# Performance work log

Measured on AMD Instinct MI355X. Metric: run time of the kernel, lower is better.

Reference implementation:

```python
import jax, jax.numpy as jnp
import numpy as np

B, C, M, H, W = 4, 12, 2, 320, 320
TOL = 1e-6
MAX_ITER = 10


def to_c(t):
    # [..., 2] real -> complex
    return jax.lax.complex(t[..., 0], t[..., 1])


def to_r(t):
    return jnp.stack([jnp.real(t), jnp.imag(t)], axis=-1)


def fft2c(x):
    return jnp.fft.fft2(x, axes=(-2, -1), norm='ortho')


def ifft2c(x):
    return jnp.fft.ifft2(x, axes=(-2, -1), norm='ortho')


def A_op(x, sm, mk):
    # x: [B,M,H,W] complex, sm: [B,C,M,H,W] complex, mk: [B,C,H,W] real
    coil_imgs = jnp.sum(x[:, None] * sm, axis=2)  # [B,C,H,W]
    return fft2c(coil_imgs) * mk


def AT_op(y, sm, mk):
    img = ifft2c(y * mk)  # [B,C,H,W]
    return jnp.sum(jnp.conj(sm) * img[:, :, None], axis=1)  # [B,M,H,W]


def cg_solve(x0, Mop, tol=TOL, max_iter=MAX_ITER):
    b = x0.shape[0]
    x0x0 = jnp.sum(jnp.abs(x0.reshape(b, -1)) ** 2, axis=-1)  # [B] real

    def body(carry, _):
        x, r, p, rr = carry
        active = jnp.min(rr / x0x0) > tol  # tol check, gated like the while-loop
        q = Mop(p)
        pq = jnp.sum((p * jnp.conj(q)).reshape(b, -1), axis=-1)  # complexDot(p, q)
        alpha = rr.astype(x0.dtype) / pq  # complex_div(rr, <p,q>)
        a = alpha[:, None, None, None]
        x_new = x + a * p
        r_new = r - a * q
        rr_new = jnp.sum(jnp.abs(r_new.reshape(b, -1)) ** 2, axis=-1)
        beta = (rr_new / rr)[:, None, None, None].astype(x0.dtype)
        p_new = r_new + beta * p
        new = (x_new, r_new, p_new, rr_new)
        carry = jax.tree.map(lambda n, o: jnp.where(active, n, o), new, carry)
        return carry, None

    rr0 = jnp.sum(jnp.abs(x0.reshape(b, -1)) ** 2, axis=-1)
    init = (jnp.zeros_like(x0), x0, x0, rr0)
    (x, _, _, _), _ = jax.lax.scan(body, init, None, length=max_iter)
    return x


def setup_inputs() -> dict:
    key = jax.random.key(0)
    k1, k2, k3, k4 = jax.random.split(key, 4)
    x = jax.random.normal(k1, (B, M, H, W, 2), dtype=jnp.float32)
    y = jax.random.normal(k2, (B, C, H, W, 2), dtype=jnp.float32)
    smaps = jax.random.normal(k3, (B, C, M, H, W, 2), dtype=jnp.float32) * 0.2
    mask = jax.random.randint(k4, (B, C, H, W, 1), 0, 2).astype(jnp.float32)
    lambda_a = jnp.full((1,), 0.05, dtype=jnp.float32)
    return {"x": x, "y": y, "smaps": smaps, "mask": mask, "lambda_a": lambda_a}


def reference(x, y, smaps, mask, lambda_a):
    z = to_c(x)          # [B,M,H,W]
    yc = to_c(y)         # [B,C,H,W]
    sm = to_c(smaps)     # [B,C,M,H,W]
    mk = mask[..., 0]    # [B,C,H,W]
    lam = lambda_a[0]

    x0 = lam * AT_op(yc, sm, mk) + z

    def Mop(p):
        return lam * AT_op(A_op(p, sm, mk), sm, mk) + p

    return to_r(cg_solve(x0, Mop))
```

## Files before the change

### kernel.cpp

```cpp
#include <hip/hip_runtime.h>
#include <math.h>

#define NB 4
#define NC 12
#define NM 2
#define NN 320
#define NHW (NN*NN)
#define NBC (NB*NC)
#define CG_TOL 1e-6f
#define NITER 10
#define CBLK 400
#define QBLK 320
#define CPG 3
#define NG  4

#define TWO_PI_F 6.28318530717958647692f

typedef float2 c32;

__device__ __forceinline__ c32 cmul(c32 a, c32 b){ return make_float2(a.x*b.x - a.y*b.y, a.x*b.y + a.y*b.x); }
__device__ __forceinline__ c32 cmulj(c32 a, c32 b){ return make_float2(a.x*b.x + a.y*b.y, a.x*b.y - a.y*b.x); }
__device__ __forceinline__ c32 cadd(c32 a, c32 b){ return make_float2(a.x+b.x, a.y+b.y); }
__device__ __forceinline__ c32 csub(c32 a, c32 b){ return make_float2(a.x-b.x, a.y-b.y); }
__device__ __forceinline__ c32 cscale(c32 a, float s){ return make_float2(a.x*s, a.y*s); }

template<bool CONJ>
__device__ __forceinline__ c32 twmul(c32 a, c32 t){
  return CONJ ? make_float2(a.x*t.x + a.y*t.y, a.y*t.x - a.x*t.y)
              : make_float2(a.x*t.x - a.y*t.y, a.y*t.x + a.x*t.y);
}

__device__ __forceinline__ float wave_reduce_f(float v) {
  #pragma unroll
  for (int off = 32; off >= 1; off >>= 1) v += __shfl_xor(v, off, 64);
  return v;
}
__device__ __forceinline__ c32 wave_reduce_c(c32 v) {
  #pragma unroll
  for (int off = 32; off >= 1; off >>= 1) {
    v.x += __shfl_xor(v.x, off, 64);
    v.y += __shfl_xor(v.y, off, 64);
  }
  return v;
}

__global__ __launch_bounds__(256)
void twiddle_init(c32* __restrict__ T320, c32* __restrict__ T64)
{
  const int t = threadIdx.x;
  {
    float s, c; sincosf(TWO_PI_F * (float)t / 320.f, &s, &c);
    T320[t] = make_float2(c, s);
  }
  if (t < 32) {
    float s, c; sincosf(TWO_PI_F * (float)t / 64.f, &s, &c);
    T64[t] = make_float2(c, s);
  }
}

template<bool FWD>
__device__ __forceinline__ void radix5(c32 V[5]) {
  constexpr float C1 = 0.30901699437494745f;
  constexpr float S1 = 0.9510565162951535f;
  constexpr float C2 = -0.8090169943749475f;
  constexpr float S2 = 0.5877852522924731f;
  constexpr float sg = FWD ? -1.f : 1.f;
  const c32 w1 = make_float2(C1,  sg*S1);
  const c32 w2 = make_float2(C2,  sg*S2);
  const c32 w3 = make_float2(C2, -sg*S2);
  const c32 w4 = make_float2(C1, -sg*S1);
  c32 v0=V[0], v1=V[1], v2=V[2], v3=V[3], v4=V[4];
  V[0] = cadd(cadd(v0, v1), cadd(cadd(v2, v3), v4));
  V[1] = cadd(v0, cadd(cadd(cmul(v1,w1), cmul(v2,w2)), cadd(cmul(v3,w3), cmul(v4,w4))));
  V[2] = cadd(v0, cadd(cadd(cmul(v1,w2), cmul(v2,w4)), cadd(cmul(v3,w1), cmul(v4,w3))));
  V[3] = cadd(v0, cadd(cadd(cmul(v1,w3), cmul(v2,w1)), cadd(cmul(v3,w4), cmul(v4,w2))));
  V[4] = cadd(v0, cadd(cadd(cmul(v1,w4), cmul(v2,w3)), cadd(cmul(v3,w2), cmul(v4,w1))));
}

template<bool FWD>
__device__ __forceinline__ void fft320_one(c32 A[5], const c32 ct[4], const c32 tw[6], int lane)
{
  radix5<FWD>(A);
  #pragma unroll
  for (int k = 1; k < 5; ++k) A[k] = twmul<FWD>(A[k], ct[k-1]);
  #pragma unroll
  for (int s = 0; s < 6; ++s) {
    const int m = 32 >> s;
    const c32 w = tw[s];
    const bool up = (lane & m) != 0;
    c32 o[5];
    #pragma unroll
    for (int k = 0; k < 5; ++k) { o[k].x = __shfl_xor(A[k].x, m, 64); o[k].y = __shfl_xor(A[k].y, m, 64); }
    #pragma unroll
    for (int k = 0; k < 5; ++k) {
      c32 lo = cadd(A[k], o[k]);
      c32 hi = twmul<FWD>(csub(o[k], A[k]), w);
      A[k] = up ? hi : lo;
    }
  }
}

__device__ __forceinline__ void ifft320_dit(c32 A[5], const c32 ct[4], const c32 tw[6], int lane)
{
  #pragma unroll
  for (int s = 5; s >= 0; --s) {
    const int m = 32 >> s;
    const c32 w = tw[s];
    const bool up = (lane & m) != 0;
    #pragma unroll
    for (int k = 0; k < 5; ++k) {
      c32 t = up ? twmul<false>(A[k], w) : A[k];
      c32 o; o.x = __shfl_xor(t.x, m, 64); o.y = __shfl_xor(t.y, m, 64);
      A[k] = up ? csub(o, t) : cadd(t, o);
    }
  }
  #pragma unroll
  for (int k = 1; k < 5; ++k) A[k] = twmul<false>(A[k], ct[k-1]);
  radix5<false>(A);
}

#define LOAD_TWIDDLES \
  c32 ct[4], tw[6]; \
  _Pragma("unroll") for (int k_ = 0; k_ < 4; ++k_) ct[k_] = T320[(k_ + 1) * lane]; \
  _Pragma("unroll") for (int s_ = 0; s_ < 6; ++s_) tw[s_] = T64[(lane & ((32 >> s_) - 1)) << s_];

__global__ __launch_bounds__(512)
void setup_mask_ifft(const c32* __restrict__ in, c32* __restrict__ out,
                     const float* __restrict__ mask,
                     const c32* __restrict__ T320, const c32* __restrict__ T64)
{
  __shared__ c32 tile[8][NN + 2];
  const int tid = threadIdx.x, lane = tid & 63, wv = tid >> 6;
  const int bc = blockIdx.y, r0 = blockIdx.x * 8;
  LOAD_TWIDDLES
  const int rv6 = __brev((unsigned)lane) >> 26;
  const int row = r0 + wv;
  c32 A[5];
  #pragma unroll
  for (int j = 0; j < 5; ++j) {
    const size_t idx = ((size_t)bc * NN + row) * NN + lane + 64*j;
    A[j] = cscale(in[idx], mask[idx]);
  }
  fft320_one<false>(A, ct, tw, lane);
  #pragma unroll
  for (int k = 0; k < 5; ++k) tile[wv][k + 5*rv6] = A[k];
  __syncthreads();
  #pragma unroll
  for (int it = 0; it < 5; ++it) {
    const int idx = it * 512 + tid, u = idx >> 3, d = idx & 7;
    out[((size_t)bc * NN + u) * NN + (r0 + d)] = tile[d][u];
  }
}

__global__ __launch_bounds__(512)
void setup_init(const c32* __restrict__ bufin, const c32* __restrict__ smaps,
                const c32* __restrict__ z, c32* __restrict__ x,
                c32* __restrict__ r, c32* __restrict__ p,
                const float* __restrict__ lam, float* __restrict__ part,
                const c32* __restrict__ T320, const c32* __restrict__ T64)
{
  __shared__ c32 tile[8][NN + 2];
  __shared__ float sredf[8];
  const int tid = threadIdx.x, lane = tid & 63, wv = tid >> 6;
  const int b = blockIdx.y, r0 = blockIdx.x * 8;
  LOAD_TWIDDLES
  const int rv6 = __brev((unsigned)lane) >> 26;
  const int w = r0 + wv;
  const float l0 = lam[0] * (1.f / (float)NN);
  c32 acc[NM][5];
  #pragma unroll
  for (int m = 0; m < NM; ++m)
    #pragma unroll
    for (int it = 0; it < 5; ++it) acc[m][it] = make_float2(0.f, 0.f);

  for (int c = 0; c < NC; ++c) {
    c32 A[5];
    #pragma unroll
    for (int j = 0; j < 5; ++j)
      A[j] = bufin[((size_t)(b*NC + c) * NN + w) * NN + lane + 64*j];
    fft320_one<false>(A, ct, tw, lane);
    __syncthreads();
    #pragma unroll
    for (int k = 0; k < 5; ++k) tile[wv][k + 5*rv6] = A[k];
    __syncthreads();
    #pragma unroll
    for (int it = 0; it < 5; ++it) {
      const int idx = it * 512 + tid, u = idx >> 3, d = idx & 7;
      c32 v = tile[d][u];
      #pragma unroll
      for (int m = 0; m < NM; ++m) {
        c32 s = smaps[(size_t)((b*NC + c)*NM + m) * NHW + (size_t)u * NN + (r0 + d)];
        acc[m][it] = cadd(acc[m][it], cmulj(s, v));
      }
    }
  }
  float accf = 0.f;
  #pragma unroll
  for (int it = 0; it < 5; ++it) {
    const int idx = it * 512 + tid, u = idx >> 3, d = idx & 7;
    #pragma unroll
    for (int m = 0; m < NM; ++m) {
      const size_t im = (size_t)(b*NM + m) * NHW + (size_t)u * NN + (r0 + d);
      c32 x0v = cadd(cscale(acc[m][it], l0), z[im]);
      x[im] = make_float2(0.f, 0.f);
      r[im] = x0v; p[im] = x0v;
      accf += x0v.x*x0v.x + x0v.y*x0v.y;
    }
  }
  accf = wave_reduce_f(accf);
  if (lane == 0) sredf[wv] = accf;
  __syncthreads();
  if (tid == 0) {
    float s = 0.f;
    #pragma unroll
    for (int k = 0; k < 8; ++k) s += sredf[k];
    part[b*CBLK + blockIdx.x] = s;
  }
}

__global__ void reduce_init(const float* __restrict__ part, float* __restrict__ x0x0,
                            float* __restrict__ rr0, float* __restrict__ flags)
{
  const int lane = threadIdx.x & 63;
  const int b = threadIdx.x >> 6;
  float s = 0.f;
  for (int j = lane; j < 40; j += 64) s += part[b*CBLK + j];
  s = wave_reduce_f(s);
  if (lane == 0) { x0x0[b] = s; rr0[b] = s; }
  if (threadIdx.x == 0) flags[0] = 1.f;
}

__global__ __launch_bounds__(512)
void fft_comb_deep(c32* __restrict__ out, const c32* __restrict__ pin,
                   const c32* __restrict__ rres, c32* __restrict__ pout,
                   const c32* __restrict__ smaps,
                   const float* __restrict__ rr_prev, const float* __restrict__ rr_cur,
                   const float* __restrict__ flag,
                   const c32* __restrict__ T320, const c32* __restrict__ T64)
{
  if (flag[0] == 0.f) return;
  __shared__ c32 tile[8][NN + 2];
  const int tid = threadIdx.x, lane = tid & 63, wv = tid >> 6;
  const int by = blockIdx.y, b = by >> 2, g = by & 3;
  const int r0 = blockIdx.x * 8;
  const int row = r0 + wv;
  const bool upd = (rr_cur != nullptr);
  const float beta = upd ? rr_cur[b] / rr_prev[b] : 0.f;
  LOAD_TWIDDLES
  const int rv6 = __brev((unsigned)lane) >> 26;
  const size_t m0 = (size_t)(b*NM + 0) * NHW, m1 = (size_t)(b*NM + 1) * NHW;
  c32 p0[5], p1[5];
  #pragma unroll
  for (int j = 0; j < 5; ++j) {
    const size_t h = (size_t)row * NN + lane + 64*j;
    c32 r0v = rres[m0 + h], r1v = rres[m1 + h];
    if (upd) {
      p0[j] = cadd(r0v, cscale(pin[m0 + h], beta));
      p1[j] = cadd(r1v, cscale(pin[m1 + h], beta));
      if (g == 0) { pout[m0 + h] = p0[j]; pout[m1 + h] = p1[j]; }
    } else { p0[j] = r0v; p1[j] = r1v; }
  }
  for (int cc = 0; cc < CPG; ++cc) {
    const int c = g * CPG + cc;
    const size_t s0o = (size_t)((b*NC + c)*NM + 0) * NHW, s1o = (size_t)((b*NC + c)*NM + 1) * NHW;
    c32 A[5];
    #pragma unroll
    for (int j = 0; j < 5; ++j) {
      const size_t h = (size_t)row * NN + lane + 64*j;
      A[j] = cadd(cmul(p0[j], smaps[s0o + h]), cmul(p1[j], smaps[s1o + h]));
    }
    fft320_one<true>(A, ct, tw, lane);
    __syncthreads();
    #pragma unroll
    for (int k = 0; k < 5; ++k) tile[wv][k + 5*rv6] = A[k];
    __syncthreads();
    #pragma unroll
    for (int it = 0; it < 5; ++it) {
      const int idx = it * 512 + tid, u = idx >> 3, d = idx & 7;
      out[(size_t)(b*NC + c) * NHW + (size_t)u * NN + (r0 + d)] = tile[d][u];
    }
  }
}

__global__ __launch_bounds__(512)
void fmi_deep(const c32* __restrict__ in, c32* __restrict__ out,
              const float* __restrict__ mask, const float* __restrict__ flag,
              const c32* __restrict__ T320, const c32* __restrict__ T64)
{
  if (flag[0] == 0.f) return;
  __shared__ c32 tile[8][NN + 2];
  const int tid = threadIdx.x, lane = tid & 63, wv = tid >> 6;
  const int by = blockIdx.y, b = by >> 2, g = by & 3;
  const int r0 = blockIdx.x * 8;
  const int row = r0 + wv;
  LOAD_TWIDDLES
  const int rv6 = __brev((unsigned)lane) >> 26;
  for (int cc = 0; cc < CPG; ++cc) {
    const int bc = b*NC + g*CPG + cc;
    c32 A[5];
    #pragma unroll
    for (int j = 0; j < 5; ++j)
      A[j] = in[((size_t)bc * NN + row) * NN + lane + 64*j];
    fft320_one<true>(A, ct, tw, lane);
    #pragma unroll
    for (int k = 0; k < 5; ++k) {
      const int kh = k + 5*rv6;
      A[k] = cscale(A[k], mask[(size_t)bc * NHW + (size_t)kh * NN + row]);
    }
    ifft320_dit(A, ct, tw, lane);
    __syncthreads();
    #pragma unroll
    for (int j = 0; j < 5; ++j) tile[wv][lane + 64*j] = A[j];
    __syncthreads();
    #pragma unroll
    for (int it = 0; it < 5; ++it) {
      const int idx = it * 512 + tid, u = idx >> 3, d = idx & 7;
      out[(size_t)bc * NHW + (size_t)u * NN + (r0 + d)] = tile[d][u];
    }
  }
}

__global__ __launch_bounds__(64)
void ifft_q(const c32* __restrict__ bufin, const c32* __restrict__ smaps,
            const c32* __restrict__ p, c32* __restrict__ q,
            const float* __restrict__ lam, const float* __restrict__ flag,
            c32* __restrict__ pqpart,
            const c32* __restrict__ T320, const c32* __restrict__ T64)
{
  if (flag[0] == 0.f) return;
  __shared__ c32 tile[NN + 2];
  const int lane = threadIdx.x;
  const int b = blockIdx.y, h = blockIdx.x;
  LOAD_TWIDDLES
  const int rv6 = __brev((unsigned)lane) >> 26;
  const float lq = lam[0] * (1.f / (float)NHW);
  const size_t rowoff = (size_t)h * NN + lane;
  c32 acc0[5], acc1[5];
  #pragma unroll
  for (int j = 0; j < 5; ++j) { acc0[j] = make_float2(0.f,0.f); acc1[j] = make_float2(0.f,0.f); }
  c32 Ac[5], S0c[5], S1c[5];
  {
    const size_t ib  = (size_t)(b*NC) * NHW + rowoff;
    const size_t is0 = (size_t)((b*NC)*NM + 0) * NHW + rowoff;
    const size_t is1 = (size_t)((b*NC)*NM + 1) * NHW + rowoff;
    #pragma unroll
    for (int j = 0; j < 5; ++j) {
      Ac[j] = bufin[ib + 64*j]; S0c[j] = smaps[is0 + 64*j]; S1c[j] = smaps[is1 + 64*j];
    }
  }
  for (int c = 0; c < NC; ++c) {
    c32 An[5], S0n[5], S1n[5];
    if (c + 1 < NC) {
      const size_t ib  = (size_t)(b*NC + c+1) * NHW + rowoff;
      const size_t is0 = (size_t)((b*NC + c+1)*NM + 0) * NHW + rowoff;
      const size_t is1 = (size_t)((b*NC + c+1)*NM + 1) * NHW + rowoff;
      #pragma unroll
      for (int j = 0; j < 5; ++j) {
        An[j] = bufin[ib + 64*j]; S0n[j] = smaps[is0 + 64*j]; S1n[j] = smaps[is1 + 64*j];
      }
    }
    fft320_one<false>(Ac, ct, tw, lane);
    #pragma unroll
    for (int k = 0; k < 5; ++k) tile[k + 5*rv6] = Ac[k];
    __syncthreads();
    #pragma unroll
    for (int j = 0; j < 5; ++j) {
      c32 v = tile[lane + 64*j];
      acc0[j] = cadd(acc0[j], cmulj(S0c[j], v));
      acc1[j] = cadd(acc1[j], cmulj(S1c[j], v));
    }
    __syncthreads();
    if (c + 1 < NC) {
      #pragma unroll
      for (int j = 0; j < 5; ++j) { Ac[j]=An[j]; S0c[j]=S0n[j]; S1c[j]=S1n[j]; }
    }
  }
  const size_t i0 = (size_t)(b*NM + 0) * NHW + rowoff;
  const size_t i1 = (size_t)(b*NM + 1) * NHW + rowoff;
  c32 pqs = make_float2(0.f, 0.f);
  #pragma unroll
  for (int j = 0; j < 5; ++j) {
    c32 p0 = p[i0 + 64*j], p1 = p[i1 + 64*j];
    c32 q0 = cadd(cscale(acc0[j], lq), p0);
    c32 q1 = cadd(cscale(acc1[j], lq), p1);
    q[i0 + 64*j] = q0; q[i1 + 64*j] = q1;
    pqs = cadd(pqs, cadd(cmulj(q0, p0), cmulj(q1, p1)));
  }
  pqs = wave_reduce_c(pqs);
  if (lane == 0) pqpart[b*QBLK + blockIdx.x] = pqs;
}

__global__ __launch_bounds__(256)
void update1(c32* __restrict__ x, c32* __restrict__ r,
             const c32* __restrict__ p, const c32* __restrict__ q,
             const float* __restrict__ rr_i, const c32* __restrict__ pqpart,
             const float* __restrict__ flag, float* __restrict__ part)
{
  if (flag[0] == 0.f) return;
  const int b = blockIdx.y;
  const int t = threadIdx.x;
  c32 s = make_float2(0.f, 0.f);
  for (int j = t; j < QBLK; j += 256) s = cadd(s, pqpart[b*QBLK + j]);
  s = wave_reduce_c(s);
  __shared__ c32 spq[4];
  const int lane = t & 63, wv = t >> 6;
  if (lane == 0) spq[wv] = s;
  __syncthreads();
  const c32 pqv = cadd(cadd(spq[0], spq[1]), cadd(spq[2], spq[3]));
  const float rrv = rr_i[b];
  const float den = pqv.x*pqv.x + pqv.y*pqv.y;
  const c32 alpha = make_float2(rrv * pqv.x / den, -rrv * pqv.y / den);
  const int hw = blockIdx.x * 256 + t;
  float acc = 0.f;
  #pragma unroll
  for (int m = 0; m < NM; ++m) {
    const size_t idx = (size_t)(b*NM + m) * NHW + hw;
    c32 pe = p[idx], qe = q[idx];
    c32 xe = cadd(x[idx], cmul(alpha, pe));
    c32 re = csub(r[idx], cmul(alpha, qe));
    x[idx] = xe; r[idx] = re;
    acc += re.x*re.x + re.y*re.y;
  }
  acc = wave_reduce_f(acc);
  __shared__ float sred[4];
  if (lane == 0) sred[wv] = acc;
  __syncthreads();
  if (t == 0) part[b*CBLK + blockIdx.x] = sred[0]+sred[1]+sred[2]+sred[3];
}

__global__ void reduce_rr(const float* __restrict__ part, const float* __restrict__ rr_i,
                          float* __restrict__ rr_n, const float* __restrict__ x0x0,
                          const float* __restrict__ flag_i, float* __restrict__ flag_n)
{
  const int lane = threadIdx.x & 63;
  const int b = threadIdx.x >> 6;
  __shared__ float sred[4];
  __shared__ float sx0[4];
  if (flag_i[0] == 0.f) {
    if (lane == 0) rr_n[b] = rr_i[b];
    if (threadIdx.x == 0) flag_n[0] = 0.f;
    return;
  }
  float s = 0.f;
  for (int j = lane; j < CBLK; j += 64) s += part[b*CBLK + j];
  s = wave_reduce_f(s);
  if (lane == 0) { rr_n[b] = s; sred[b] = s; sx0[b] = x0x0[b]; }
  __syncthreads();
  if (threadIdx.x == 0) {
    float mn = 1e30f;
    #pragma unroll
    for (int bb = 0; bb < NB; ++bb) mn = fminf(mn, sred[bb] / sx0[bb]);
    flag_n[0] = (mn > CG_TOL) ? 1.f : 0.f;
  }
}

extern "C" void kernel_launch(void* const* d_in, const int* in_sizes, int n_in,
                              void* d_out, int out_size, void* d_ws, size_t ws_size,
                              hipStream_t stream)
{
  const c32*  z   = (const c32*)d_in[0];
  const c32*  y   = (const c32*)d_in[1];
  const c32*  sm  = (const c32*)d_in[2];
  const float* mk = (const float*)d_in[3];
  const float* lam= (const float*)d_in[4];
  c32* x = (c32*)d_out;

  char* base = (char*)d_ws;
  size_t off = 0;
  auto walloc = [&](size_t bytes) -> void* {
    void* ptr = base + off;
    off += (bytes + 255) & ~(size_t)255;
    return ptr;
  };
  c32* buf1   = (c32*)walloc((size_t)NBC * NHW * sizeof(c32));
  c32* buf2   = (c32*)walloc((size_t)NBC * NHW * sizeof(c32));
  c32* rv     = (c32*)walloc((size_t)NB * NM * NHW * sizeof(c32));
  c32* pvA    = (c32*)walloc((size_t)NB * NM * NHW * sizeof(c32));
  c32* pvB    = (c32*)walloc((size_t)NB * NM * NHW * sizeof(c32));
  c32* qv     = (c32*)walloc((size_t)NB * NM * NHW * sizeof(c32));
  c32* pqpart = (c32*)walloc((size_t)NB * QBLK * sizeof(c32));
  float* x0x0 = (float*)walloc(NB * sizeof(float));
  float* rr   = (float*)walloc((NITER + 1) * NB * sizeof(float));
  float* flags= (float*)walloc((NITER + 1) * sizeof(float));
  float* part1= (float*)walloc((size_t)NB * CBLK * sizeof(float));
  c32* T320   = (c32*)walloc(256 * sizeof(c32));
  c32* T64    = (c32*)walloc(32 * sizeof(c32));
  (void)ws_size; (void)in_sizes; (void)n_in; (void)out_size;

  dim3 blk512(512), blk256(256), blk64(64);
  dim3 sgrid1(NN / 8, NBC);
  dim3 sgrid2(NN / 8, NB);
  dim3 dgrid(NN / 8, NB * NG);
  dim3 qgrid(QBLK, NB);
  dim3 ugrid(CBLK, NB);

  twiddle_init<<<1, blk256, 0, stream>>>(T320, T64);

  setup_mask_ifft<<<sgrid1, blk512, 0, stream>>>(y, buf2, mk, T320, T64);
  setup_init<<<sgrid2, blk512, 0, stream>>>(buf2, sm, z, x, rv, pvA, lam, part1, T320, T64);
  reduce_init<<<1, blk256, 0, stream>>>(part1, x0x0, rr, flags);

  for (int i = 0; i < NITER; ++i) {
    const float* fl = flags + i;
    c32* pin  = (i & 1) ? pvA : pvB;
    c32* pout = (i & 1) ? pvB : pvA;
    const float* rrprev = (i > 0) ? (rr + (i-1)*NB) : rr;
    const float* rrcur  = (i > 0) ? (rr + i*NB) : nullptr;
    fft_comb_deep<<<dgrid, blk512, 0, stream>>>(buf2, pin, rv, pout, sm, rrprev, rrcur, fl, T320, T64);
    fmi_deep<<<dgrid, blk512, 0, stream>>>(buf2, buf1, mk, fl, T320, T64);
    ifft_q<<<qgrid, blk64, 0, stream>>>(buf1, sm, pout, qv, lam, fl, pqpart, T320, T64);
    update1<<<ugrid, blk256, 0, stream>>>(x, rv, pout, qv, rr + i*NB, pqpart, fl, part1);
    reduce_rr<<<1, blk256, 0, stream>>>(part1, rr + i*NB, rr + (i+1)*NB, x0x0, fl, flags + (i+1));
  }
}
```

Baseline: 406.5 us.

## Split setup across coil groups and fold CG reductions into FFT kernel

The setup adjoint now splits the coil sum across four groups, so it launches four times as many blocks. A new elementwise setup_fin kernel sums the per-group partials, initializes x, r and p, and computes the rr partials. The separate reduce_init and reduce_rr kernels are removed. Each fft_comb_deep block now redundantly reduces the rr partials, computes beta and the convergence flag itself, and writes rr and flags for later kernels. This trades an extra partial-accumulator buffer pass and redundant small reductions per block for better GPU occupancy in setup and fewer serialized launches per CG iteration.

```diff
diff --git a/kernel.cpp b/kernel.cpp
--- a/kernel.cpp
+++ b/kernel.cpp
@@ -9,7 +9,7 @@
 #define NBC (NB*NC)
 #define CG_TOL 1e-6f
 #define NITER 10
-#define CBLK 400
+#define PBLK 400
 #define QBLK 320
 #define CPG 3
 #define NG  4
@@ -131,49 +131,50 @@
 {
   __shared__ c32 tile[8][NN + 2];
   const int tid = threadIdx.x, lane = tid & 63, wv = tid >> 6;
-  const int bc = blockIdx.y, r0 = blockIdx.x * 8;
+  const int by = blockIdx.y, b = by >> 2, g = by & 3;
+  const int r0 = blockIdx.x * 8;
+  const int row = r0 + wv;
   LOAD_TWIDDLES
   const int rv6 = __brev((unsigned)lane) >> 26;
-  const int row = r0 + wv;
-  c32 A[5];
-  #pragma unroll
-  for (int j = 0; j < 5; ++j) {
-    const size_t idx = ((size_t)bc * NN + row) * NN + lane + 64*j;
-    A[j] = cscale(in[idx], mask[idx]);
-  }
-  fft320_one<false>(A, ct, tw, lane);
-  #pragma unroll
-  for (int k = 0; k < 5; ++k) tile[wv][k + 5*rv6] = A[k];
-  __syncthreads();
-  #pragma unroll
-  for (int it = 0; it < 5; ++it) {
-    const int idx = it * 512 + tid, u = idx >> 3, d = idx & 7;
-    out[((size_t)bc * NN + u) * NN + (r0 + d)] = tile[d][u];
+  for (int cc = 0; cc < CPG; ++cc) {
+    const int bc = b*NC + g*CPG + cc;
+    c32 A[5];
+    #pragma unroll
+    for (int j = 0; j < 5; ++j) {
+      const size_t idx = ((size_t)bc * NN + row) * NN + lane + 64*j;
+      A[j] = cscale(in[idx], mask[idx]);
+    }
+    fft320_one<false>(A, ct, tw, lane);
+    __syncthreads();
+    #pragma unroll
+    for (int k = 0; k < 5; ++k) tile[wv][k + 5*rv6] = A[k];
+    __syncthreads();
+    #pragma unroll
+    for (int it = 0; it < 5; ++it) {
+      const int idx = it * 512 + tid, u = idx >> 3, d = idx & 7;
+      out[((size_t)bc * NN + u) * NN + (r0 + d)] = tile[d][u];
+    }
   }
 }
 
 __global__ __launch_bounds__(512)
 void setup_init(const c32* __restrict__ bufin, const c32* __restrict__ smaps,
-                const c32* __restrict__ z, c32* __restrict__ x,
-                c32* __restrict__ r, c32* __restrict__ p,
-                const float* __restrict__ lam, float* __restrict__ part,
+                c32* __restrict__ pacc,
                 const c32* __restrict__ T320, const c32* __restrict__ T64)
 {
   __shared__ c32 tile[8][NN + 2];
-  __shared__ float sredf[8];
   const int tid = threadIdx.x, lane = tid & 63, wv = tid >> 6;
-  const int b = blockIdx.y, r0 = blockIdx.x * 8;
+  const int by = blockIdx.y, b = by >> 2, g = by & 3;
+  const int r0 = blockIdx.x * 8;
+  const int w = r0 + wv;
   LOAD_TWIDDLES
   const int rv6 = __brev((unsigned)lane) >> 26;
-  const int w = r0 + wv;
-  const float l0 = lam[0] * (1.f / (float)NN);
-  c32 acc[NM][5];
-  #pragma unroll
-  for (int m = 0; m < NM; ++m)
-    #pragma unroll
-    for (int it = 0; it < 5; ++it) acc[m][it] = make_float2(0.f, 0.f);
-
-  for (int c = 0; c < NC; ++c) {
+  c32 acc0[5], acc1[5];
+  #pragma unroll
+  for (int it = 0; it < 5; ++it) { acc0[it] = make_float2(0.f,0.f); acc1[it] = make_float2(0.f,0.f); }
+
+  for (int cc = 0; cc < CPG; ++cc) {
+    const int c = g*CPG + cc;
     c32 A[5];
     #pragma unroll
     for (int j = 0; j < 5; ++j)
@@ -187,65 +188,84 @@
     for (int it = 0; it < 5; ++it) {
       const int idx = it * 512 + tid, u = idx >> 3, d = idx & 7;
       c32 v = tile[d][u];
-      #pragma unroll
-      for (int m = 0; m < NM; ++m) {
-        c32 s = smaps[(size_t)((b*NC + c)*NM + m) * NHW + (size_t)u * NN + (r0 + d)];
-        acc[m][it] = cadd(acc[m][it], cmulj(s, v));
-      }
-    }
-  }
-  float accf = 0.f;
+      c32 s0 = smaps[(size_t)((b*NC + c)*NM + 0) * NHW + (size_t)u * NN + (r0 + d)];
+      c32 s1 = smaps[(size_t)((b*NC + c)*NM + 1) * NHW + (size_t)u * NN + (r0 + d)];
+      acc0[it] = cadd(acc0[it], cmulj(s0, v));
+      acc1[it] = cadd(acc1[it], cmulj(s1, v));
+    }
+  }
   #pragma unroll
   for (int it = 0; it < 5; ++it) {
     const int idx = it * 512 + tid, u = idx >> 3, d = idx & 7;
-    #pragma unroll
-    for (int m = 0; m < NM; ++m) {
-      const size_t im = (size_t)(b*NM + m) * NHW + (size_t)u * NN + (r0 + d);
-      c32 x0v = cadd(cscale(acc[m][it], l0), z[im]);
-      x[im] = make_float2(0.f, 0.f);
-      r[im] = x0v; p[im] = x0v;
-      accf += x0v.x*x0v.x + x0v.y*x0v.y;
-    }
+    const size_t hw = (size_t)u * NN + (r0 + d);
+    pacc[(size_t)((g*NB + b)*NM + 0) * NHW + hw] = acc0[it];
+    pacc[(size_t)((g*NB + b)*NM + 1) * NHW + hw] = acc1[it];
+  }
+}
+
+__global__ __launch_bounds__(256)
+void setup_fin(const c32* __restrict__ pacc, const c32* __restrict__ z,
+               c32* __restrict__ x, c32* __restrict__ r, c32* __restrict__ p,
+               const float* __restrict__ lam, float* __restrict__ part)
+{
+  const int b  = blockIdx.y;
+  const int hw = blockIdx.x * 256 + threadIdx.x;
+  const float l0 = lam[0] * (1.f / (float)NN);
+  float accf = 0.f;
+  #pragma unroll
+  for (int m = 0; m < NM; ++m) {
+    c32 a = make_float2(0.f, 0.f);
+    #pragma unroll
+    for (int g = 0; g < NG; ++g)
+      a = cadd(a, pacc[(size_t)((g*NB + b)*NM + m) * NHW + hw]);
+    const size_t im = (size_t)(b*NM + m) * NHW + hw;
+    c32 x0v = cadd(cscale(a, l0), z[im]);
+    x[im] = make_float2(0.f, 0.f);
+    r[im] = x0v; p[im] = x0v;
+    accf += x0v.x*x0v.x + x0v.y*x0v.y;
   }
   accf = wave_reduce_f(accf);
-  if (lane == 0) sredf[wv] = accf;
+  __shared__ float sred[4];
+  const int lane = threadIdx.x & 63, wv = threadIdx.x >> 6;
+  if (lane == 0) sred[wv] = accf;
   __syncthreads();
-  if (tid == 0) {
-    float s = 0.f;
-    #pragma unroll
-    for (int k = 0; k < 8; ++k) s += sredf[k];
-    part[b*CBLK + blockIdx.x] = s;
-  }
-}
-
-__global__ void reduce_init(const float* __restrict__ part, float* __restrict__ x0x0,
-                            float* __restrict__ rr0, float* __restrict__ flags)
-{
-  const int lane = threadIdx.x & 63;
-  const int b = threadIdx.x >> 6;
-  float s = 0.f;
-  for (int j = lane; j < 40; j += 64) s += part[b*CBLK + j];
-  s = wave_reduce_f(s);
-  if (lane == 0) { x0x0[b] = s; rr0[b] = s; }
-  if (threadIdx.x == 0) flags[0] = 1.f;
+  if (threadIdx.x == 0) part[b*PBLK + blockIdx.x] = sred[0]+sred[1]+sred[2]+sred[3];
 }
 
 __global__ __launch_bounds__(512)
 void fft_comb_deep(c32* __restrict__ out, const c32* __restrict__ pin,
                    const c32* __restrict__ rres, c32* __restrict__ pout,
                    const c32* __restrict__ smaps,
-                   const float* __restrict__ rr_prev, const float* __restrict__ rr_cur,
-                   const float* __restrict__ flag,
+                   float* __restrict__ rr, float* __restrict__ flags,
+                   const float* __restrict__ part1, const int it,
                    const c32* __restrict__ T320, const c32* __restrict__ T64)
 {
-  if (flag[0] == 0.f) return;
   __shared__ c32 tile[8][NN + 2];
+  __shared__ float sstat[NB];
   const int tid = threadIdx.x, lane = tid & 63, wv = tid >> 6;
   const int by = blockIdx.y, b = by >> 2, g = by & 3;
   const int r0 = blockIdx.x * 8;
   const int row = r0 + wv;
-  const bool upd = (rr_cur != nullptr);
-  const float beta = upd ? rr_cur[b] / rr_prev[b] : 0.f;
+  if (wv < NB) {
+    float s = 0.f;
+    for (int j = lane; j < PBLK; j += 64) s += part1[wv*PBLK + j];
+    s = wave_reduce_f(s);
+    if (lane == 0) sstat[wv] = s;
+  }
+  __syncthreads();
+  float flag;
+  if (it == 0) flag = 1.f;
+  else {
+    float mn = 1e30f;
+    #pragma unroll
+    for (int bb = 0; bb < NB; ++bb) mn = fminf(mn, sstat[bb] / rr[bb]);
+    flag = (mn > CG_TOL) ? 1.f : 0.f;
+  }
+  if (tid < NB) rr[it*NB + tid] = sstat[tid];
+  if (tid == 0) flags[it] = flag;
+  if (it != 0 && flag == 0.f) return;
+  const float beta = (it != 0) ? sstat[b] / rr[(it-1)*NB + b] : 0.f;
+
   LOAD_TWIDDLES
   const int rv6 = __brev((unsigned)lane) >> 26;
   const size_t m0 = (size_t)(b*NM + 0) * NHW, m1 = (size_t)(b*NM + 1) * NHW;
@@ -254,7 +274,7 @@
   for (int j = 0; j < 5; ++j) {
     const size_t h = (size_t)row * NN + lane + 64*j;
     c32 r0v = rres[m0 + h], r1v = rres[m1 + h];
-    if (upd) {
+    if (it != 0) {
       p0[j] = cadd(r0v, cscale(pin[m0 + h], beta));
       p1[j] = cadd(r1v, cscale(pin[m1 + h], beta));
       if (g == 0) { pout[m0 + h] = p0[j]; pout[m1 + h] = p1[j]; }
@@ -275,8 +295,8 @@
     for (int k = 0; k < 5; ++k) tile[wv][k + 5*rv6] = A[k];
     __syncthreads();
     #pragma unroll
-    for (int it = 0; it < 5; ++it) {
-      const int idx = it * 512 + tid, u = idx >> 3, d = idx & 7;
+    for (int itr = 0; itr < 5; ++itr) {
+      const int idx = itr * 512 + tid, u = idx >> 3, d = idx & 7;
       out[(size_t)(b*NC + c) * NHW + (size_t)u * NN + (r0 + d)] = tile[d][u];
     }
   }
@@ -393,8 +413,9 @@
 __global__ __launch_bounds__(256)
 void update1(c32* __restrict__ x, c32* __restrict__ r,
              const c32* __restrict__ p, const c32* __restrict__ q,
-             const float* __restrict__ rr_i, const c32* __restrict__ pqpart,
-             const float* __restrict__ flag, float* __restrict__ part)
+             const float* __restrict__ rr, const c32* __restrict__ pqpart,
+             const float* __restrict__ flag, float* __restrict__ part,
+             const int it)
 {
   if (flag[0] == 0.f) return;
   const int b = blockIdx.y;
@@ -407,7 +428,7 @@
   if (lane == 0) spq[wv] = s;
   __syncthreads();
   const c32 pqv = cadd(cadd(spq[0], spq[1]), cadd(spq[2], spq[3]));
-  const float rrv = rr_i[b];
+  const float rrv = rr[it*NB + b];
   const float den = pqv.x*pqv.x + pqv.y*pqv.y;
   const c32 alpha = make_float2(rrv * pqv.x / den, -rrv * pqv.y / den);
   const int hw = blockIdx.x * 256 + t;
@@ -425,33 +446,7 @@
   __shared__ float sred[4];
   if (lane == 0) sred[wv] = acc;
   __syncthreads();
-  if (t == 0) part[b*CBLK + blockIdx.x] = sred[0]+sred[1]+sred[2]+sred[3];
-}
-
-__global__ void reduce_rr(const float* __restrict__ part, const float* __restrict__ rr_i,
-                          float* __restrict__ rr_n, const float* __restrict__ x0x0,
-                          const float* __restrict__ flag_i, float* __restrict__ flag_n)
-{
-  const int lane = threadIdx.x & 63;
-  const int b = threadIdx.x >> 6;
-  __shared__ float sred[4];
-  __shared__ float sx0[4];
-  if (flag_i[0] == 0.f) {
-    if (lane == 0) rr_n[b] = rr_i[b];
-    if (threadIdx.x == 0) flag_n[0] = 0.f;
-    return;
-  }
-  float s = 0.f;
-  for (int j = lane; j < CBLK; j += 64) s += part[b*CBLK + j];
-  s = wave_reduce_f(s);
-  if (lane == 0) { rr_n[b] = s; sred[b] = s; sx0[b] = x0x0[b]; }
-  __syncthreads();
-  if (threadIdx.x == 0) {
-    float mn = 1e30f;
-    #pragma unroll
-    for (int bb = 0; bb < NB; ++bb) mn = fminf(mn, sred[bb] / sx0[bb]);
-    flag_n[0] = (mn > CG_TOL) ? 1.f : 0.f;
-  }
+  if (t == 0) part[b*PBLK + blockIdx.x] = sred[0]+sred[1]+sred[2]+sred[3];
 }
 
 extern "C" void kernel_launch(void* const* d_in, const int* in_sizes, int n_in,
@@ -479,37 +474,31 @@
   c32* pvB    = (c32*)walloc((size_t)NB * NM * NHW * sizeof(c32));
   c32* qv     = (c32*)walloc((size_t)NB * NM * NHW * sizeof(c32));
   c32* pqpart = (c32*)walloc((size_t)NB * QBLK * sizeof(c32));
-  float* x0x0 = (float*)walloc(NB * sizeof(float));
   float* rr   = (float*)walloc((NITER + 1) * NB * sizeof(float));
   float* flags= (float*)walloc((NITER + 1) * sizeof(float));
-  float* part1= (float*)walloc((size_t)NB * CBLK * sizeof(float));
+  float* part1= (float*)walloc((size_t)NB * PBLK * sizeof(float));
   c32* T320   = (c32*)walloc(256 * sizeof(c32));
   c32* T64    = (c32*)walloc(32 * sizeof(c32));
+  c32* pacc   = buf1;
   (void)ws_size; (void)in_sizes; (void)n_in; (void)out_size;
 
   dim3 blk512(512), blk256(256), blk64(64);
-  dim3 sgrid1(NN / 8, NBC);
-  dim3 sgrid2(NN / 8, NB);
   dim3 dgrid(NN / 8, NB * NG);
+  dim3 fgrid(PBLK, NB);
   dim3 qgrid(QBLK, NB);
-  dim3 ugrid(CBLK, NB);
 
   twiddle_init<<<1, blk256, 0, stream>>>(T320, T64);
 
-  setup_mask_ifft<<<sgrid1, blk512, 0, stream>>>(y, buf2, mk, T320, T64);
-  setup_init<<<sgrid2, blk512, 0, stream>>>(buf2, sm, z, x, rv, pvA, lam, part1, T320, T64);
-  reduce_init<<<1, blk256, 0, stream>>>(part1, x0x0, rr, flags);
+  setup_mask_ifft<<<dgrid, blk512, 0, stream>>>(y, buf2, mk, T320, T64);
+  setup_init<<<dgrid, blk512, 0, stream>>>(buf2, sm, pacc, T320, T64);
+  setup_fin<<<fgrid, blk256, 0, stream>>>(pacc, z, x, rv, pvA, lam, part1);
 
   for (int i = 0; i < NITER; ++i) {
-    const float* fl = flags + i;
     c32* pin  = (i & 1) ? pvA : pvB;
     c32* pout = (i & 1) ? pvB : pvA;
-    const float* rrprev = (i > 0) ? (rr + (i-1)*NB) : rr;
-    const float* rrcur  = (i > 0) ? (rr + i*NB) : nullptr;
-    fft_comb_deep<<<dgrid, blk512, 0, stream>>>(buf2, pin, rv, pout, sm, rrprev, rrcur, fl, T320, T64);
-    fmi_deep<<<dgrid, blk512, 0, stream>>>(buf2, buf1, mk, fl, T320, T64);
-    ifft_q<<<qgrid, blk64, 0, stream>>>(buf1, sm, pout, qv, lam, fl, pqpart, T320, T64);
-    update1<<<ugrid, blk256, 0, stream>>>(x, rv, pout, qv, rr + i*NB, pqpart, fl, part1);
-    reduce_rr<<<1, blk256, 0, stream>>>(part1, rr + i*NB, rr + (i+1)*NB, x0x0, fl, flags + (i+1));
-  }
-}
+    fft_comb_deep<<<dgrid, blk512, 0, stream>>>(buf2, pin, rv, pout, sm, rr, flags, part1, i, T320, T64);
+    fmi_deep<<<dgrid, blk512, 0, stream>>>(buf2, buf1, mk, flags + i, T320, T64);
+    ifft_q<<<qgrid, blk64, 0, stream>>>(buf1, sm, pout, qv, lam, flags + i, pqpart, T320, T64);
+    update1<<<fgrid, blk256, 0, stream>>>(x, rv, pout, qv, rr, pqpart, flags + i, part1, i);
+  }
+}
```

After: 419.4 us. +3.2%, slower.
